# Performance work log

Measured on AMD Instinct MI355X. Metric: run time of the kernel, lower is better.

The kernel has to match this reference:

```python
import jax, jax.numpy as jnp
import numpy as np

H = 10          # hidden_dim
OUT = 100       # linear output (charset logits)
STEPS = 30      # decoder steps
START = 1.0     # Alphabet.start_integer
NL = 3          # num_layers
B, L, TD, AD = 8192, 32, 63, 1
IN = TD + AD


def setup_inputs() -> dict:
    key = jax.random.key(0)
    ks = iter(jax.random.split(key, 64))
    s = 0.3
    d = {}
    d["families"] = jnp.zeros((B,), jnp.int32)
    d["languages"] = jnp.zeros((B,), jnp.int32)
    d["tags"] = jax.random.uniform(next(ks), (B, TD), jnp.float32)
    d["lemmata"] = jax.random.uniform(next(ks), (B, L), jnp.float32)
    for pre in ("enc", "dec"):
        for l in range(NL):
            din = IN if l == 0 else H
            d[f"{pre}_W_ih{l}"] = jax.random.normal(next(ks), (4 * H, din), jnp.float32) * s
            d[f"{pre}_W_hh{l}"] = jax.random.normal(next(ks), (4 * H, H), jnp.float32) * s
            d[f"{pre}_b_ih{l}"] = jax.random.normal(next(ks), (4 * H,), jnp.float32) * s
            d[f"{pre}_b_hh{l}"] = jax.random.normal(next(ks), (4 * H,), jnp.float32) * s
    d["lin_W"] = jax.random.normal(next(ks), (OUT, H), jnp.float32) * s
    d["lin_b"] = jnp.zeros((OUT,), jnp.float32)
    return d


def _lstm_cell(layers, h, c, x):
    # torch LSTM gate order: i, f, g, o. Dropout inactive in eval mode.
    nh, nc, inp = [], [], x
    for (W_ih, W_hh, b_ih, b_hh), hl, cl in zip(layers, h, c):
        g = inp @ W_ih.T + hl @ W_hh.T + b_ih + b_hh  # (B, 4H)
        i_, f_, g_, o_ = jnp.split(g, 4, axis=-1)
        cl = jax.nn.sigmoid(f_) * cl + jax.nn.sigmoid(i_) * jnp.tanh(g_)
        hl = jax.nn.sigmoid(o_) * jnp.tanh(cl)
        nh.append(hl); nc.append(cl); inp = hl
    return tuple(nh), tuple(nc), inp


def _forward(tags, lemmata, enc, dec, lin_W, lin_b):
    Bb, Ll = lemmata.shape
    # time-major encoder input: feature order [char, tags...] -> (L, B, 1+TD)
    xs = jnp.concatenate([lemmata.T[:, :, None],
                          jnp.broadcast_to(tags[None], (Ll, Bb, tags.shape[1]))], axis=-1)
    h = tuple(jnp.zeros((Bb, H), lemmata.dtype) for _ in range(NL))
    c = h

    def estep(carry, x):
        hh, cc = carry
        hh, cc, _ = _lstm_cell(enc, hh, cc, x)
        return (hh, cc), None

    (h, c), _ = jax.lax.scan(estep, (h, c), xs)

    tok = jnp.full((Bb,), START, lemmata.dtype)

    def dstep(carry, _):
        hh, cc, t = carry
        x = jnp.concatenate([t[:, None], tags], axis=-1)  # (B, 1+TD)
        hh, cc, y = _lstm_cell(dec, hh, cc, x)
        probs = jax.nn.sigmoid(y @ lin_W.T + lin_b)       # (B, 100)
        nt = jax.lax.stop_gradient(jnp.argmax(probs, axis=-1))
        return (hh, cc, nt.astype(t.dtype)), (probs, nt)

    _, (probs, toks) = jax.lax.scan(dstep, (h, c, tok), None, length=STEPS)
    return jnp.transpose(probs, (1, 0, 2)), toks.T  # (B,30,100), (B,30)


def reference(families, languages, tags, lemmata,
              enc_W_ih0, enc_W_hh0, enc_b_ih0, enc_b_hh0,
              enc_W_ih1, enc_W_hh1, enc_b_ih1, enc_b_hh1,
              enc_W_ih2, enc_W_hh2, enc_b_ih2, enc_b_hh2,
              dec_W_ih0, dec_W_hh0, dec_b_ih0, dec_b_hh0,
              dec_W_ih1, dec_W_hh1, dec_b_ih1, dec_b_hh1,
              dec_W_ih2, dec_W_hh2, dec_b_ih2, dec_b_hh2,
              lin_W, lin_b):
    enc = ((enc_W_ih0, enc_W_hh0, enc_b_ih0, enc_b_hh0),
           (enc_W_ih1, enc_W_hh1, enc_b_ih1, enc_b_hh1),
           (enc_W_ih2, enc_W_hh2, enc_b_ih2, enc_b_hh2))
    dec = ((dec_W_ih0, dec_W_hh0, dec_b_ih0, dec_b_hh0),
           (dec_W_ih1, dec_W_hh1, dec_b_ih1, dec_b_hh1),
           (dec_W_ih2, dec_W_hh2, dec_b_ih2, dec_b_hh2))
    return _forward(tags, lemmata, enc, dec, lin_W, lin_b)
```

## Files before the change

kernel.cpp:

```cpp
#include <hip/hip_runtime.h>
#include <cmath>
#include <stdint.h>

#define DEV __device__ __forceinline__

typedef float v2f __attribute__((ext_vector_type(2)));

static DEV float fast_exp2(float x) { return __builtin_amdgcn_exp2f(x); }
static DEV float fast_rcp(float x) { return __builtin_amdgcn_rcpf(x); }

#define LOG2E 1.4426950408889634f

static DEV float rdl(float x, int l) {
  return __int_as_float(__builtin_amdgcn_readlane(__float_as_int(x), l));
}
static DEV int rdli(float x, int l) {
  return __builtin_amdgcn_readlane(__float_as_int(x), l);
}
static DEV uint64_t pack2(int lo, int hi) {
  return ((uint64_t)(uint32_t)hi << 32) | (uint32_t)lo;
}

static DEV void pkfma(v2f& acc, v2f w, uint64_t h) {
  asm("v_pk_fma_f32 %0, %1, %2, %0" : "+v"(acc) : "v"(w), "s"(h));
}

template <int K>
static DEV float qb(float x) {
  return __int_as_float(
      __builtin_amdgcn_update_dpp(0, __float_as_int(x), K * 0x55, 0xF, 0xF, true));
}

template <int CTRL>
static DEV float dppmax(float x) {
  float o = __int_as_float(
      __builtin_amdgcn_update_dpp(0, __float_as_int(x), CTRL, 0xF, 0xF, true));
  return fmaxf(x, o);
}

static DEV float wavemax_bcast(float m) {
  m = dppmax<0x111>(m);
  m = dppmax<0x112>(m);
  m = dppmax<0x114>(m);
  m = dppmax<0x118>(m);
  m = dppmax<0x142>(m);
  m = dppmax<0x143>(m);
  return rdl(m, 63);
}

struct KP {
  const float* tags; const float* lem;
  const float* eWih0; const float* eWhh0; const float* ebih0; const float* ebhh0;
  const float* eWih1; const float* eWhh1; const float* ebih1; const float* ebhh1;
  const float* eWih2; const float* eWhh2; const float* ebih2; const float* ebhh2;
  const float* dWih0; const float* dWhh0; const float* dbih0; const float* dbhh0;
  const float* dWih1; const float* dWhh1; const float* dbih1; const float* dbhh1;
  const float* dWih2; const float* dWhh2; const float* dbih2; const float* dbhh2;
  const float* linW; const float* linb;
  float* outp; float* outt;
  int B;
};

__global__ __launch_bounds__(256) void seq2seq_kernel(KP P) {
  const int tid = threadIdx.x;
  const int lane = tid & 63;
  const int b = blockIdx.x * 4 + (tid >> 6);
  if (b >= P.B) return;

  const int jq = lane >> 2;
  const int kg = lane & 3;
  const int jj = (jq < 10) ? jq : 9;
  const int row = kg * 10 + jj;

  const float kc = (kg == 2) ? (-2.0f * LOG2E) : (-LOG2E);
  const float am = (kg == 2) ? 2.0f : 1.0f;
  const float ab = (kg == 2) ? -1.0f : 0.0f;

  auto act = [&](float g) -> float {
    float y = fast_rcp(1.0f + fast_exp2(g * kc));
    return fmaf(am, y, ab);
  };

  float tv = (lane < 63) ? P.tags[(size_t)b * 63 + lane] : 0.0f;
  float lemv = (lane < 32) ? P.lem[(size_t)b * 32 + lane] : 0.0f;

  float pre0 = P.ebih0[row] + P.ebhh0[row];
  float dpre0 = P.dbih0[row] + P.dbhh0[row];
  float ew0c, dw0c;
  {
    const float4* e4 = (const float4*)P.eWih0 + row * 16;
    const float4* d4 = (const float4*)P.dWih0 + row * 16;
    float4 we = e4[0], wd = d4[0];
    ew0c = we.x; dw0c = wd.x;
    float t0 = rdl(tv, 0), t1 = rdl(tv, 1), t2 = rdl(tv, 2);
    pre0 = fmaf(we.y, t0, pre0); pre0 = fmaf(we.z, t1, pre0); pre0 = fmaf(we.w, t2, pre0);
    dpre0 = fmaf(wd.y, t0, dpre0); dpre0 = fmaf(wd.z, t1, dpre0); dpre0 = fmaf(wd.w, t2, dpre0);
#pragma unroll
    for (int c = 1; c < 16; c++) {
      float4 e = e4[c], d = d4[c];
      int dd = 4 * c - 1;
      float u0 = rdl(tv, dd), u1 = rdl(tv, dd + 1), u2 = rdl(tv, dd + 2), u3 = rdl(tv, dd + 3);
      pre0 = fmaf(e.x, u0, pre0); pre0 = fmaf(e.y, u1, pre0);
      pre0 = fmaf(e.z, u2, pre0); pre0 = fmaf(e.w, u3, pre0);
      dpre0 = fmaf(d.x, u0, dpre0); dpre0 = fmaf(d.y, u1, dpre0);
      dpre0 = fmaf(d.z, u2, dpre0); dpre0 = fmaf(d.w, u3, dpre0);
    }
  }

  v2f ehh0[5], eih1[5], ehh1[5], eih2[5], ehh2[5];
  {
    const v2f* a0 = (const v2f*)(P.eWhh0 + row * 10);
    const v2f* a1 = (const v2f*)(P.eWih1 + row * 10);
    const v2f* a2 = (const v2f*)(P.eWhh1 + row * 10);
    const v2f* a3 = (const v2f*)(P.eWih2 + row * 10);
    const v2f* a4 = (const v2f*)(P.eWhh2 + row * 10);
#pragma unroll
    for (int q = 0; q < 5; q++) {
      ehh0[q] = a0[q]; eih1[q] = a1[q]; ehh1[q] = a2[q];
      eih2[q] = a3[q]; ehh2[q] = a4[q];
    }
  }
  float pre1 = P.ebih1[row] + P.ebhh1[row];
  float pre2 = P.ebih2[row] + P.ebhh2[row];

  uint64_t h0[5], h1[5], h2[5];
#pragma unroll
  for (int q = 0; q < 5; q++) { h0[q] = 0; h1[q] = 0; h2[q] = 0; }
  float c0 = 0.0f, c1 = 0.0f, c2 = 0.0f;

  auto upd = [&](float a, float& c, uint64_t (&h)[5]) {
    float a0 = qb<0>(a);
    float a1 = qb<1>(a);
    float a2 = qb<2>(a);
    float a3 = qb<3>(a);
    c = fmaf(a1, c, a0 * a2);
    float y = fast_rcp(1.0f + fast_exp2(c * (-2.0f * LOG2E)));
    float hv = a3 * fmaf(2.0f, y, -1.0f);
#pragma unroll
    for (int q = 0; q < 5; q++) h[q] = pack2(rdli(hv, 8 * q), rdli(hv, 8 * q + 4));
  };

  auto step = [&](float x, const v2f (&wh0)[5], const v2f (&wi1)[5],
                  const v2f (&wh1)[5], const v2f (&wi2)[5], const v2f (&wh2)[5],
                  float w0c, float p0_, float p1_, float p2_) {
    v2f s0{p0_, 0.0f}, s1{p1_, 0.0f}, s2{p2_, 0.0f};
#pragma unroll
    for (int q = 0; q < 5; q++) {
      pkfma(s0, wh0[q], h0[q]);
      pkfma(s1, wh1[q], h1[q]);
      pkfma(s2, wh2[q], h2[q]);
    }
    upd(act(fmaf(w0c, x, s0.x + s0.y)), c0, h0);

    v2f t1{0.0f, 0.0f};
#pragma unroll
    for (int q = 0; q < 5; q++) pkfma(t1, wi1[q], h0[q]);
    upd(act((s1.x + s1.y) + (t1.x + t1.y)), c1, h1);

    v2f t2{0.0f, 0.0f};
#pragma unroll
    for (int q = 0; q < 5; q++) pkfma(t2, wi2[q], h1[q]);
    upd(act((s2.x + s2.y) + (t2.x + t2.y)), c2, h2);
  };

#pragma unroll 2
  for (int t = 0; t < 32; t++) {
    step(rdl(lemv, t), ehh0, eih1, ehh1, eih2, ehh2, ew0c, pre0, pre1, pre2);
  }

  {
    const v2f* a0 = (const v2f*)(P.dWhh0 + row * 10);
    const v2f* a1 = (const v2f*)(P.dWih1 + row * 10);
    const v2f* a2 = (const v2f*)(P.dWhh1 + row * 10);
    const v2f* a3 = (const v2f*)(P.dWih2 + row * 10);
    const v2f* a4 = (const v2f*)(P.dWhh2 + row * 10);
#pragma unroll
    for (int q = 0; q < 5; q++) {
      ehh0[q] = a0[q]; eih1[q] = a1[q]; ehh1[q] = a2[q];
      eih2[q] = a3[q]; ehh2[q] = a4[q];
    }
  }
  pre1 = P.dbih1[row] + P.dbhh1[row];
  pre2 = P.dbih2[row] + P.dbhh2[row];

  const int lr2 = (lane < 36) ? (64 + lane) : 99;
  v2f lw0[5], lw1[5];
  {
    const v2f* a0 = (const v2f*)(P.linW + lane * 10);
    const v2f* a1 = (const v2f*)(P.linW + lr2 * 10);
#pragma unroll
    for (int q = 0; q < 5; q++) { lw0[q] = a0[q]; lw1[q] = a1[q]; }
  }
  float lb0 = P.linb[lane];
  float lb1 = (lane < 36) ? P.linb[lr2] : -1e30f;

  float* op0 = P.outp + (size_t)b * 3000;
  float tok = 1.0f;
  float tokv = 0.0f;

#pragma unroll 2
  for (int s = 0; s < 30; s++) {
    step(tok, ehh0, eih1, ehh1, eih2, ehh2, dw0c, dpre0, pre1, pre2);

    v2f za{lb0, 0.0f}, zb{lb1, 0.0f};
#pragma unroll
    for (int q = 0; q < 5; q++) { pkfma(za, lw0[q], h2[q]); pkfma(zb, lw1[q], h2[q]); }
    float z0 = za.x + za.y, z1 = zb.x + zb.y;
    float p0 = fast_rcp(1.0f + fast_exp2(z0 * (-LOG2E)));
    float p1 = fast_rcp(1.0f + fast_exp2(z1 * (-LOG2E)));

    float* op = op0 + s * 100;
    op[lane] = p0;
    if (lane < 36) op[64 + lane] = p1;

    float vm = wavemax_bcast(fmaxf(p0, p1));
    unsigned long long m0 = __ballot(p0 == vm);
    unsigned long long m1 = __ballot(p1 == vm);
    int im = m0 ? (int)__builtin_ctzll(m0) : 64 + (int)__builtin_ctzll(m1);
    tok = (float)im;
    tokv = (lane == s) ? tok : tokv;
  }

  if (lane < 30) P.outt[(size_t)b * 30 + lane] = tokv;
}

extern "C" void kernel_launch(void* const* d_in, const int* in_sizes, int n_in,
                              void* d_out, int out_size, void* d_ws, size_t ws_size,
                              hipStream_t stream) {
  KP P;
  P.tags = (const float*)d_in[2];
  P.lem = (const float*)d_in[3];
  P.eWih0 = (const float*)d_in[4];  P.eWhh0 = (const float*)d_in[5];
  P.ebih0 = (const float*)d_in[6];  P.ebhh0 = (const float*)d_in[7];
  P.eWih1 = (const float*)d_in[8];  P.eWhh1 = (const float*)d_in[9];
  P.ebih1 = (const float*)d_in[10]; P.ebhh1 = (const float*)d_in[11];
  P.eWih2 = (const float*)d_in[12]; P.eWhh2 = (const float*)d_in[13];
  P.ebih2 = (const float*)d_in[14]; P.ebhh2 = (const float*)d_in[15];
  P.dWih0 = (const float*)d_in[16]; P.dWhh0 = (const float*)d_in[17];
  P.dbih0 = (const float*)d_in[18]; P.dbhh0 = (const float*)d_in[19];
  P.dWih1 = (const float*)d_in[20]; P.dWhh1 = (const float*)d_in[21];
  P.dbih1 = (const float*)d_in[22]; P.dbhh1 = (const float*)d_in[23];
  P.dWih2 = (const float*)d_in[24]; P.dWhh2 = (const float*)d_in[25];
  P.dbih2 = (const float*)d_in[26]; P.dbhh2 = (const float*)d_in[27];
  P.linW = (const float*)d_in[28];
  P.linb = (const float*)d_in[29];

  const int B = in_sizes[3] / 32;
  P.B = B;
  P.outp = (float*)d_out;
  P.outt = P.outp + (size_t)B * 3000;

  const int blocks = (B + 3) / 4;
  seq2seq_kernel<<<dim3(blocks), dim3(256), 0, stream>>>(P);
}
```

Baseline: 150.3 us.

## Prescale weights by activation constants and hoist decoder recurrent dots off the token path

Folds the sigmoid/tanh exponent scale factors (-log2e, -2log2e) into the LSTM and linear weights and biases at load time, which removes a multiply before each exp2. It also splits the layer-1/2 input dot products into two independent accumulators to shorten dependency chains. In the decoder, the recurrent h@W_hh products for the next step are computed right after the state update, overlapping them with the output projection and argmax, so only the token-dependent term waits on the argmax. Rounding changes slightly, which could flip argmax ties.

```diff
diff --git a/kernel.cpp b/kernel.cpp
--- a/kernel.cpp
+++ b/kernel.cpp
@@ -77,7 +77,7 @@
   const float ab = (kg == 2) ? -1.0f : 0.0f;
 
   auto act = [&](float g) -> float {
-    float y = fast_rcp(1.0f + fast_exp2(g * kc));
+    float y = fast_rcp(1.0f + fast_exp2(g));
     return fmaf(am, y, ab);
   };
 
@@ -105,6 +105,7 @@
       dpre0 = fmaf(d.x, u0, dpre0); dpre0 = fmaf(d.y, u1, dpre0);
       dpre0 = fmaf(d.z, u2, dpre0); dpre0 = fmaf(d.w, u3, dpre0);
     }
+    pre0 *= kc; dpre0 *= kc; ew0c *= kc; dw0c *= kc;
   }
 
   v2f ehh0[5], eih1[5], ehh1[5], eih2[5], ehh2[5];
@@ -116,12 +117,12 @@
     const v2f* a4 = (const v2f*)(P.eWhh2 + row * 10);
 #pragma unroll
     for (int q = 0; q < 5; q++) {
-      ehh0[q] = a0[q]; eih1[q] = a1[q]; ehh1[q] = a2[q];
-      eih2[q] = a3[q]; ehh2[q] = a4[q];
-    }
-  }
-  float pre1 = P.ebih1[row] + P.ebhh1[row];
-  float pre2 = P.ebih2[row] + P.ebhh2[row];
+      ehh0[q] = a0[q] * kc; eih1[q] = a1[q] * kc; ehh1[q] = a2[q] * kc;
+      eih2[q] = a3[q] * kc; ehh2[q] = a4[q] * kc;
+    }
+  }
+  float pre1 = (P.ebih1[row] + P.ebhh1[row]) * kc;
+  float pre2 = (P.ebih2[row] + P.ebhh2[row]) * kc;
 
   uint64_t h0[5], h1[5], h2[5];
 #pragma unroll
@@ -140,33 +141,29 @@
     for (int q = 0; q < 5; q++) h[q] = pack2(rdli(hv, 8 * q), rdli(hv, 8 * q + 4));
   };
 
-  auto step = [&](float x, const v2f (&wh0)[5], const v2f (&wi1)[5],
-                  const v2f (&wh1)[5], const v2f (&wi2)[5], const v2f (&wh2)[5],
-                  float w0c, float p0_, float p1_, float p2_) {
-    v2f s0{p0_, 0.0f}, s1{p1_, 0.0f}, s2{p2_, 0.0f};
-#pragma unroll
-    for (int q = 0; q < 5; q++) {
-      pkfma(s0, wh0[q], h0[q]);
-      pkfma(s1, wh1[q], h1[q]);
-      pkfma(s2, wh2[q], h2[q]);
-    }
-    upd(act(fmaf(w0c, x, s0.x + s0.y)), c0, h0);
-
-    v2f t1{0.0f, 0.0f};
-#pragma unroll
-    for (int q = 0; q < 5; q++) pkfma(t1, wi1[q], h0[q]);
-    upd(act((s1.x + s1.y) + (t1.x + t1.y)), c1, h1);
-
-    v2f t2{0.0f, 0.0f};
-#pragma unroll
-    for (int q = 0; q < 5; q++) pkfma(t2, wi2[q], h1[q]);
-    upd(act((s2.x + s2.y) + (t2.x + t2.y)), c2, h2);
+  auto tdot = [&](const v2f (&w)[5], const uint64_t (&h)[5]) -> float {
+    v2f ta{0.0f, 0.0f}, tb{0.0f, 0.0f};
+    pkfma(ta, w[0], h[0]); pkfma(tb, w[1], h[1]);
+    pkfma(ta, w[2], h[2]); pkfma(tb, w[3], h[3]);
+    pkfma(ta, w[4], h[4]);
+    return (ta.x + ta.y) + (tb.x + tb.y);
+  };
+
+  auto step = [&](float x) {
+    v2f s0{pre0, 0.0f}, s1{pre1, 0.0f}, s2{pre2, 0.0f};
+#pragma unroll
+    for (int q = 0; q < 5; q++) {
+      pkfma(s0, ehh0[q], h0[q]);
+      pkfma(s1, ehh1[q], h1[q]);
+      pkfma(s2, ehh2[q], h2[q]);
+    }
+    upd(act(fmaf(ew0c, x, s0.x + s0.y)), c0, h0);
+    upd(act((s1.x + s1.y) + tdot(eih1, h0)), c1, h1);
+    upd(act((s2.x + s2.y) + tdot(eih2, h1)), c2, h2);
   };
 
 #pragma unroll 2
-  for (int t = 0; t < 32; t++) {
-    step(rdl(lemv, t), ehh0, eih1, ehh1, eih2, ehh2, ew0c, pre0, pre1, pre2);
-  }
+  for (int t = 0; t < 32; t++) step(rdl(lemv, t));
 
   {
     const v2f* a0 = (const v2f*)(P.dWhh0 + row * 10);
@@ -176,12 +173,12 @@
     const v2f* a4 = (const v2f*)(P.dWhh2 + row * 10);
 #pragma unroll
     for (int q = 0; q < 5; q++) {
-      ehh0[q] = a0[q]; eih1[q] = a1[q]; ehh1[q] = a2[q];
-      eih2[q] = a3[q]; ehh2[q] = a4[q];
-    }
-  }
-  pre1 = P.dbih1[row] + P.dbhh1[row];
-  pre2 = P.dbih2[row] + P.dbhh2[row];
+      ehh0[q] = a0[q] * kc; eih1[q] = a1[q] * kc; ehh1[q] = a2[q] * kc;
+      eih2[q] = a3[q] * kc; ehh2[q] = a4[q] * kc;
+    }
+  }
+  pre1 = (P.dbih1[row] + P.dbhh1[row]) * kc;
+  pre2 = (P.dbih2[row] + P.dbhh2[row]) * kc;
 
   const int lr2 = (lane < 36) ? (64 + lane) : 99;
   v2f lw0[5], lw1[5];
@@ -189,25 +186,42 @@
     const v2f* a0 = (const v2f*)(P.linW + lane * 10);
     const v2f* a1 = (const v2f*)(P.linW + lr2 * 10);
 #pragma unroll
-    for (int q = 0; q < 5; q++) { lw0[q] = a0[q]; lw1[q] = a1[q]; }
-  }
-  float lb0 = P.linb[lane];
-  float lb1 = (lane < 36) ? P.linb[lr2] : -1e30f;
+    for (int q = 0; q < 5; q++) { lw0[q] = a0[q] * (-LOG2E); lw1[q] = a1[q] * (-LOG2E); }
+  }
+  float lb0 = P.linb[lane] * (-LOG2E);
+  float lb1 = ((lane < 36) ? P.linb[lr2] : -1e30f) * (-LOG2E);
 
   float* op0 = P.outp + (size_t)b * 3000;
   float tok = 1.0f;
   float tokv = 0.0f;
 
+  v2f sp0{dpre0, 0.0f}, sp1{pre1, 0.0f}, sp2{pre2, 0.0f};
+#pragma unroll
+  for (int q = 0; q < 5; q++) {
+    pkfma(sp0, ehh0[q], h0[q]);
+    pkfma(sp1, ehh1[q], h1[q]);
+    pkfma(sp2, ehh2[q], h2[q]);
+  }
+
 #pragma unroll 2
   for (int s = 0; s < 30; s++) {
-    step(tok, ehh0, eih1, ehh1, eih2, ehh2, dw0c, dpre0, pre1, pre2);
+    upd(act(fmaf(dw0c, tok, sp0.x + sp0.y)), c0, h0);
+    upd(act((sp1.x + sp1.y) + tdot(eih1, h0)), c1, h1);
+    upd(act((sp2.x + sp2.y) + tdot(eih2, h1)), c2, h2);
+
+    sp0 = v2f{dpre0, 0.0f}; sp1 = v2f{pre1, 0.0f}; sp2 = v2f{pre2, 0.0f};
+#pragma unroll
+    for (int q = 0; q < 5; q++) {
+      pkfma(sp0, ehh0[q], h0[q]);
+      pkfma(sp1, ehh1[q], h1[q]);
+      pkfma(sp2, ehh2[q], h2[q]);
+    }
 
     v2f za{lb0, 0.0f}, zb{lb1, 0.0f};
 #pragma unroll
     for (int q = 0; q < 5; q++) { pkfma(za, lw0[q], h2[q]); pkfma(zb, lw1[q], h2[q]); }
-    float z0 = za.x + za.y, z1 = zb.x + zb.y;
-    float p0 = fast_rcp(1.0f + fast_exp2(z0 * (-LOG2E)));
-    float p1 = fast_rcp(1.0f + fast_exp2(z1 * (-LOG2E)));
+    float p0 = fast_rcp(1.0f + fast_exp2(za.x + za.y));
+    float p1 = fast_rcp(1.0f + fast_exp2(zb.x + zb.y));
 
     float* op = op0 + s * 100;
     op[lane] = p0;
```

Measured after the change: 151.8 us. Within noise of the previous version (+1.0%).
